# Kernel tuning notes

Hardware: AMD Instinct MI355X
Metric: run time of the kernel (lower is better)

## Reference

```python
import jax, jax.numpy as jnp
import numpy as np

# longformer-base-4096 config
L, H, D, DH, FF = 12, 12, 768, 64, 3072
B, S, W = 1, 4096, 256            # W = one-sided attention window (attention_window 512)
V, MAXP, NCLS = 50265, 4098, 6
NC = S // W                        # number of chunks of size W


def layer_norm(x, s, b, eps=1e-5):
    m = jnp.mean(x, -1, keepdims=True)
    v = jnp.var(x, -1, keepdims=True)
    return (x - m) * jax.lax.rsqrt(v + eps) * s + b


def sliding_attn(q, k, v, kv_mask):
    # q,k,v: [B,H,S,DH]; kv_mask: [B,S] float (1=keep, 0=pad)
    qc = q.reshape(B, H, NC, W, DH)
    pad = ((0, 0), (0, 0), (W, W), (0, 0))
    kp = jnp.pad(k, pad).reshape(B, H, NC + 2, W, DH)
    vp = jnp.pad(v, pad).reshape(B, H, NC + 2, W, DH)
    # each chunk c sees key chunks c-1, c, c+1 -> [B,H,NC,3W,DH]
    k3 = jnp.concatenate([kp[:, :, i:i + NC] for i in range(3)], axis=3)
    v3 = jnp.concatenate([vp[:, :, i:i + NC] for i in range(3)], axis=3)
    scores = jnp.einsum('bhcqd,bhckd->bhcqk', qc, k3) / np.float32(np.sqrt(DH))
    # banded mask: |key_global - query_global| <= W  <=>  qi <= kj <= qi + 2W
    qi = jnp.arange(W)[:, None]
    kj = jnp.arange(3 * W)[None, :]
    band = (kj >= qi) & (kj <= qi + 2 * W)                       # [W,3W]
    mp = jnp.pad(kv_mask, ((0, 0), (W, W))).reshape(B, NC + 2, W)
    m3 = jnp.concatenate([mp[:, i:i + NC] for i in range(3)], axis=2)  # [B,NC,3W]
    allowed = band[None, None, None] & (m3[:, None, :, None, :] > 0)
    probs = jax.nn.softmax(jnp.where(allowed, scores, -1e9), axis=-1)
    out = jnp.einsum('bhcqk,bhckd->bhcqd', probs, v3)            # [B,H,NC,W,DH]
    return out.reshape(B, H, S, DH)


def setup_inputs():
    ki = iter(jax.random.split(jax.random.key(0), 16))
    p = lambda sh: 0.02 * jax.random.normal(next(ki), sh, jnp.float32)
    ids = jax.random.randint(next(ki), (B, S), 0, V, dtype=jnp.int32)
    mask = jnp.ones((B, S), jnp.int32)
    return dict(
        ids=ids, mask=mask,
        word_emb=p((V, D)), pos_emb=p((MAXP, D)), type_emb=p((D,)),
        ln_e_s=jnp.ones((D,), jnp.float32), ln_e_b=jnp.zeros((D,), jnp.float32),
        wq=p((L, D, D)), bq=jnp.zeros((L, D), jnp.float32),
        wk=p((L, D, D)), bk=jnp.zeros((L, D), jnp.float32),
        wv=p((L, D, D)), bv=jnp.zeros((L, D), jnp.float32),
        wo=p((L, D, D)), bo=jnp.zeros((L, D), jnp.float32),
        ln1_s=jnp.ones((L, D), jnp.float32), ln1_b=jnp.zeros((L, D), jnp.float32),
        w1=p((L, D, FF)), b1=jnp.zeros((L, FF), jnp.float32),
        w2=p((L, FF, D)), b2=jnp.zeros((L, D), jnp.float32),
        ln2_s=jnp.ones((L, D), jnp.float32), ln2_b=jnp.zeros((L, D), jnp.float32),
        w_pool=p((D, D)), b_pool=jnp.zeros((D,), jnp.float32),
        w_cls=p((D, NCLS)), b_cls=jnp.zeros((NCLS,), jnp.float32))


def reference(ids, mask, word_emb, pos_emb, type_emb, ln_e_s, ln_e_b,
              wq, bq, wk, bk, wv, bv, wo, bo, ln1_s, ln1_b,
              w1, b1, w2, b2, ln2_s, ln2_b, w_pool, b_pool, w_cls, b_cls):
    maskf = mask.astype(jnp.float32)
    # RoBERTa-style position ids with padding_idx=1
    pos = (jnp.cumsum(mask, axis=1) * mask + 1).astype(jnp.int32)
    x = word_emb[ids] + pos_emb[pos] + type_emb               # [B,S,D]
    x = layer_norm(x, ln_e_s, ln_e_b)

    def heads(y, w, b):
        return (y @ w + b).reshape(B, S, H, DH).transpose(0, 2, 1, 3)

    for l in range(L):
        q = heads(x, wq[l], bq[l])
        k = heads(x, wk[l], bk[l])
        v = heads(x, wv[l], bv[l])
        a = sliding_attn(q, k, v, maskf)                      # [B,H,S,DH]
        a = a.transpose(0, 2, 1, 3).reshape(B, S, D)
        x = layer_norm(x + (a @ wo[l] + bo[l]), ln1_s[l], ln1_b[l])
        h = jax.nn.gelu(x @ w1[l] + b1[l], approximate=False)
        x = layer_norm(x + (h @ w2[l] + b2[l]), ln2_s[l], ln2_b[l])

    pooled = jnp.tanh(x[:, 0] @ w_pool + b_pool)              # [B,D] pooler
    # Dropout(0.3) is identity in eval mode
    return pooled @ w_cls + b_cls                             # [B,6]
```

## Files before the change

### kernel.cpp

```cpp
#include <hip/hip_runtime.h>
#include <stdint.h>
#include <math.h>

#define NL 12
#define SQ 4096
#define DM 768
#define NH 12
#define DHD 64
#define FF 3072
#define WW 256

typedef unsigned short u16;
typedef __attribute__((ext_vector_type(8))) short bf8_t;
typedef __attribute__((ext_vector_type(4))) short s16x4;
typedef __attribute__((ext_vector_type(4))) float f4;

__device__ __forceinline__ float bf2f(u16 h) {
  union { unsigned int u; float f; } c; c.u = ((unsigned int)h) << 16; return c.f;
}
__device__ __forceinline__ u16 f2bf(float f) {
  union { float f; unsigned int u; } c; c.f = f; unsigned int u = c.u;
  return (u16)((u + 0x7fffu + ((u >> 16) & 1u)) >> 16);
}
__device__ __forceinline__ int iclamp(int v, int lo, int hi) {
  return v < lo ? lo : (v > hi ? hi : v);
}
__device__ __forceinline__ void gload16(const void* g, void* l) {
  __builtin_amdgcn_global_load_lds(
      (const __attribute__((address_space(1))) void*)g,
      (__attribute__((address_space(3))) void*)l, 16, 0, 0);
}

__global__ __launch_bounds__(256) void scan_kernel(const int* __restrict__ mask,
                                                   int* __restrict__ pos) {
  __shared__ int part[256];
  int tid = threadIdx.x;
  int base = tid * 16, ssum = 0;
  for (int i = 0; i < 16; ++i) ssum += mask[base + i];
  part[tid] = ssum;
  __syncthreads();
  if (tid == 0) {
    int run = 0;
    for (int i = 0; i < 256; ++i) { int t = part[i]; part[i] = run; run += t; }
  }
  __syncthreads();
  int run = part[tid];
  for (int i = 0; i < 16; ++i) {
    int m = mask[base + i];
    run += m;
    pos[base + i] = run * m + 1;
  }
}

__device__ __forceinline__ void block_ln4(int row, f4 a, bool act,
    const float* __restrict__ s, const float* __restrict__ b,
    float* __restrict__ xo, u16* __restrict__ xh, float* red, int tid) {
  float s1 = 0.f, s2 = 0.f;
  if (act) {
#pragma unroll
    for (int j = 0; j < 4; ++j) { s1 += a[j]; s2 += a[j] * a[j]; }
  }
#pragma unroll
  for (int m = 1; m < 64; m <<= 1) { s1 += __shfl_xor(s1, m); s2 += __shfl_xor(s2, m); }
  if ((tid & 63) == 0) { red[tid >> 6] = s1; red[4 + (tid >> 6)] = s2; }
  __syncthreads();
  s1 = red[0] + red[1] + red[2] + red[3];
  s2 = red[4] + red[5] + red[6] + red[7];
  float mean = s1 * (1.f / DM);
  float var = s2 * (1.f / DM) - mean * mean;
  float inv = rsqrtf(var + 1e-5f);
  if (act) {
    const f4 sv = ((const f4*)s)[tid];
    const f4 bv = ((const f4*)b)[tid];
    f4 y;
    s16x4 hh;
#pragma unroll
    for (int j = 0; j < 4; ++j) {
      y[j] = (a[j] - mean) * inv * sv[j] + bv[j];
      hh[j] = (short)f2bf(y[j]);
    }
    ((f4*)xo)[(size_t)row * 192 + tid] = y;
    *(s16x4*)&xh[(size_t)row * DM + tid * 4] = hh;
  }
}

__global__ __launch_bounds__(256) void embed_kernel(const int* __restrict__ ids,
    const int* __restrict__ pos, const float* __restrict__ we,
    const float* __restrict__ pe, const float* __restrict__ te,
    const float* __restrict__ s, const float* __restrict__ b,
    float* __restrict__ xo, u16* __restrict__ xh) {
  __shared__ float red[8];
  int row = blockIdx.x, tid = threadIdx.x;
  bool act = tid < 192;
  f4 a = { 0.f, 0.f, 0.f, 0.f };
  if (act) {
    int id = ids[row], pz = pos[row];
    const f4 wv = ((const f4*)we)[(size_t)id * 192 + tid];
    const f4 pv = ((const f4*)pe)[(size_t)pz * 192 + tid];
    const f4 tv = ((const f4*)te)[tid];
#pragma unroll
    for (int j = 0; j < 4; ++j) a[j] = wv[j] + pv[j] + tv[j];
  }
  block_ln4(row, a, act, s, b, xo, xh, red, tid);
}

__global__ __launch_bounds__(256) void ln_direct_kernel(
    const float* __restrict__ in, float* __restrict__ x, u16* __restrict__ xh,
    const float* __restrict__ s, const float* __restrict__ b) {
  __shared__ float red[8];
  int row = blockIdx.x, tid = threadIdx.x;
  bool act = tid < 192;
  f4 a = { 0.f, 0.f, 0.f, 0.f };
  if (act) a = ((const f4*)in)[(size_t)row * 192 + tid];
  block_ln4(row, a, act, s, b, x, xh, red, tid);
}

__global__ __launch_bounds__(256) void ln_fuse_kernel(
    const float* __restrict__ pp, int nparts, const float* __restrict__ bias,
    float* __restrict__ x, u16* __restrict__ xh,
    const float* __restrict__ s, const float* __restrict__ b) {
  __shared__ float red[8];
  int row = blockIdx.x, tid = threadIdx.x;
  bool act = tid < 192;
  f4 a = { 0.f, 0.f, 0.f, 0.f };
  if (act) {
    size_t i4 = (size_t)row * 192 + tid;
    a = ((const f4*)x)[i4];
    const f4 bb = ((const f4*)bias)[tid];
#pragma unroll
    for (int j = 0; j < 4; ++j) a[j] += bb[j];
    for (int p = 0; p < nparts; ++p) {
      const f4 pv = ((const f4*)pp)[(size_t)p * SQ * 192 + i4];
#pragma unroll
      for (int j = 0; j < 4; ++j) a[j] += pv[j];
    }
  }
  block_ln4(row, a, act, s, b, x, xh, red, tid);
}

__global__ __launch_bounds__(256) void wconv_all(
    const float* __restrict__ wq, const float* __restrict__ wk,
    const float* __restrict__ wv, const float* __restrict__ wo,
    const float* __restrict__ w1, const float* __restrict__ w2,
    u16* __restrict__ Wqkv, u16* __restrict__ Wo,
    u16* __restrict__ W1, u16* __restrict__ W2) {
  __shared__ float t[64 * 65];
  int b = blockIdx.x;
  int lay = blockIdx.y;
  const float* src;
  u16* dst;
  int K, N, rowoff, nx, tile;
  if (b < 216) {
    int j = b / 72;
    tile = b - j * 72;
    src = ((j == 0) ? wq : ((j == 1) ? wk : wv)) + (size_t)lay * DM * DM;
    dst = Wqkv + (size_t)lay * 3 * DM * DM;
    K = DM; N = DM; rowoff = j * DM; nx = 12;
  } else if (b < 288) {
    tile = b - 216;
    src = wo + (size_t)lay * DM * DM; dst = Wo + (size_t)lay * DM * DM;
    K = DM; N = DM; rowoff = 0; nx = 12;
  } else if (b < 576) {
    tile = b - 288;
    src = w1 + (size_t)lay * DM * FF; dst = W1 + (size_t)lay * DM * FF;
    K = DM; N = FF; rowoff = 0; nx = 48;
  } else {
    tile = b - 576;
    src = w2 + (size_t)lay * FF * DM; dst = W2 + (size_t)lay * FF * DM;
    K = FF; N = DM; rowoff = 0; nx = 12;
  }
  int n0 = (tile % nx) * 64, k0 = (tile / nx) * 128;
  int tid = threadIdx.x;
  int q = tid & 15, kr = tid >> 4;

  f4 v0[4], v1[4];
#pragma unroll
  for (int p = 0; p < 4; ++p)
    v0[p] = *(const f4*)&src[(size_t)(k0 + kr + p * 16) * N + n0 + q * 4];
#pragma unroll
  for (int p = 0; p < 4; ++p)
    v1[p] = *(const f4*)&src[(size_t)(k0 + 64 + kr + p * 16) * N + n0 + q * 4];

#pragma unroll
  for (int p = 0; p < 4; ++p) {
    int k = kr + p * 16;
#pragma unroll
    for (int j = 0; j < 4; ++j) t[k * 65 + q * 4 + j] = v0[p][j];
  }
  __syncthreads();
  {
    int n = tid >> 4, kq = (tid & 15) * 4;
#pragma unroll
    for (int c = 0; c < 4; ++c) {
      int nn = n + c * 16;
      s16x4 st;
#pragma unroll
      for (int i = 0; i < 4; ++i)
        st[i] = (short)f2bf(t[(kq + i) * 65 + nn]);
      *(s16x4*)&dst[(size_t)(rowoff + n0 + nn) * K + k0 + kq] = st;
    }
  }
  __syncthreads();
#pragma unroll
  for (int p = 0; p < 4; ++p) {
    int k = kr + p * 16;
#pragma unroll
    for (int j = 0; j < 4; ++j) t[k * 65 + q * 4 + j] = v1[p][j];
  }
  __syncthreads();
  {
    int n = tid >> 4, kq = (tid & 15) * 4;
#pragma unroll
    for (int c = 0; c < 4; ++c) {
      int nn = n + c * 16;
      s16x4 st;
#pragma unroll
      for (int i = 0; i < 4; ++i)
        st[i] = (short)f2bf(t[(kq + i) * 65 + nn]);
      *(s16x4*)&dst[(size_t)(rowoff + n0 + nn) * K + k0 + 64 + kq] = st;
    }
  }
}

template <int EPI>
__global__ __launch_bounds__(256, 3) void gemm1(
    const u16* __restrict__ A, const u16* __restrict__ B, int Kld, int ksl,
    int nx, int ntiles,
    const float* __restrict__ bias0, const float* __restrict__ bias1,
    const float* __restrict__ bias2, const float* __restrict__ resid,
    float* __restrict__ outf, u16* __restrict__ oh,
    u16* __restrict__ Qb, u16* __restrict__ Kb, u16* __restrict__ VTb) {
  __shared__ __align__(16) char smem[49152];

  const int tid = threadIdx.x;
  const int l = tid & 63;
  const int w = tid >> 6;
  const int lr = l & 15;
  const int lg = l >> 4;
  const int nwg = gridDim.x;
  const int bid = blockIdx.x;
  const int wg = (bid & 7) * (nwg >> 3) + (bid >> 3);
  const int part = wg / ntiles;
  const int t = wg - part * ntiles;
  const int bm = (t / nx) * 128;
  const int bn = (t % nx) * 64;
  const int k0 = part * ksl;
  const int wr = (w >> 1) * 64;
  const int wc = (w & 1) * 32;

  f4 acc[4][2];
  f4 z = { 0.f, 0.f, 0.f, 0.f };
#pragma unroll
  for (int i = 0; i < 4; ++i)
#pragma unroll
    for (int j = 0; j < 2; ++j) acc[i][j] = z;

  const int srow = tid >> 3;
  const int scol = ((tid & 7) * 8) ^ ((srow & 7) * 8);
  const int xw = (lr & 7) * 8;

  const int nkt = ksl >> 6;

  auto stage = [&](int slot, int kt) {
    int ksrc = k0 + (kt << 6);
    char* la = smem + slot * 24576 + (size_t)(tid & ~63) * 16;
    char* lb = la + 16384;
#pragma unroll
    for (int r = 0; r < 4; ++r)
      gload16(A + (size_t)(bm + srow + r * 32) * Kld + ksrc + scol, la + r * 4096);
#pragma unroll
    for (int r = 0; r < 2; ++r)
      gload16(B + (size_t)(bn + srow + r * 32) * Kld + ksrc + scol, lb + r * 4096);
  };

  stage(0, 0);
  stage(1, 1);
  asm volatile("s_waitcnt vmcnt(6)" ::: "memory");
  __builtin_amdgcn_s_barrier();
  __builtin_amdgcn_sched_barrier(0);

  for (int kt = 0; kt < nkt; ++kt) {
    const int cur = kt & 1;
    const u16* sA = (const u16*)(smem + cur * 24576);
    const u16* sB = sA + 8192;
#pragma unroll
    for (int ks = 0; ks < 2; ++ks) {
      bf8_t af[4], bfr[2];
#pragma unroll
      for (int mt = 0; mt < 4; ++mt)
        af[mt] = *(const bf8_t*)&sA[(wr + mt * 16 + lr) * 64 + ((ks * 32 + lg * 8) ^ xw)];
#pragma unroll
      for (int nt = 0; nt < 2; ++nt)
        bfr[nt] = *(const bf8_t*)&sB[(wc + nt * 16 + lr) * 64 + ((ks * 32 + lg * 8) ^ xw)];
#pragma unroll
      for (int mt = 0; mt < 4; ++mt)
#pragma unroll
        for (int nt = 0; nt < 2; ++nt)
          acc[mt][nt] = __builtin_amdgcn_mfma_f32_16x16x32_bf16(af[mt], bfr[nt], acc[mt][nt], 0, 0, 0);
    }
    asm volatile("s_waitcnt lgkmcnt(0)" ::: "memory");
    __builtin_amdgcn_sched_barrier(0);
    __builtin_amdgcn_s_barrier();
    if (kt + 2 < nkt) {
      stage(cur, kt + 2);
      asm volatile("s_waitcnt vmcnt(6)" ::: "memory");
    } else {
      asm volatile("s_waitcnt vmcnt(0)" ::: "memory");
    }
    __builtin_amdgcn_s_barrier();
    __builtin_amdgcn_sched_barrier(0);
  }
  __syncthreads();

  if constexpr (EPI == 3 || EPI == 4) {
#pragma unroll
    for (int mt = 0; mt < 4; ++mt)
#pragma unroll
      for (int nt = 0; nt < 2; ++nt) {
        int colg = bn + wc + nt * 16 + lr;
#pragma unroll
        for (int r = 0; r < 4; ++r) {
          int rowg = bm + wr + mt * 16 + lg * 4 + r;
          size_t idx = (size_t)rowg * DM + colg;
          if constexpr (EPI == 3) {
            outf[(size_t)part * SQ * DM + idx] = acc[mt][nt][r];
          } else {
            outf[idx] = acc[mt][nt][r] + bias0[colg] + resid[idx];
          }
        }
      }
    return;
  }

  float* ep = (float*)(smem + w * 9216);
  const int nbase = bn + wc;

  if constexpr (EPI == 0) {
    int tgt = nbase / DM;
    int within = nbase - tgt * DM;
    int head = within >> 6;
    const float* bp = (tgt == 0) ? bias0 : ((tgt == 1) ? bias1 : bias2);
    if (tgt == 2) {
#pragma unroll
      for (int mt = 0; mt < 4; ++mt)
#pragma unroll
        for (int nt = 0; nt < 2; ++nt) {
          int dh = (within & 63) + nt * 16 + lr;
          float bb = bp[within + nt * 16 + lr];
          int s0 = bm + wr + mt * 16 + lg * 4;
          s16x4 st;
#pragma unroll
          for (int r = 0; r < 4; ++r) st[r] = (short)f2bf(acc[mt][nt][r] + bb);
          *(s16x4*)&VTb[((size_t)(head * DHD + dh)) * SQ + s0] = st;
        }
    } else {
      u16* dst = (tgt == 0) ? Qb : Kb;
      float scale = (tgt == 0) ? 0.125f : 1.0f;
#pragma unroll
      for (int mt = 0; mt < 4; ++mt)
#pragma unroll
        for (int nt = 0; nt < 2; ++nt)
#pragma unroll
          for (int r = 0; r < 4; ++r)
            ep[(mt * 16 + lg * 4 + r) * 36 + nt * 16 + lr] = acc[mt][nt][r];
      asm volatile("s_waitcnt lgkmcnt(0)" ::: "memory");
      int coloff = (l & 7) * 4;
#pragma unroll
      for (int i = 0; i < 8; ++i) {
        int row = (l >> 3) + i * 8;
        int gs = bm + wr + row;
        f4 v = *(f4*)&ep[row * 36 + coloff];
        s16x4 st;
#pragma unroll
        for (int j = 0; j < 4; ++j)
          st[j] = (short)f2bf((v[j] + bp[within + coloff + j]) * scale);
        *(s16x4*)&dst[((size_t)head * SQ + gs) * DHD + (within & 63) + coloff] = st;
      }
    }
  } else {
#pragma unroll
    for (int mt = 0; mt < 4; ++mt)
#pragma unroll
      for (int nt = 0; nt < 2; ++nt)
#pragma unroll
        for (int r = 0; r < 4; ++r)
          ep[(mt * 16 + lg * 4 + r) * 36 + nt * 16 + lr] = acc[mt][nt][r];
    asm volatile("s_waitcnt lgkmcnt(0)" ::: "memory");
    int coloff = (l & 7) * 4;
#pragma unroll
    for (int i = 0; i < 8; ++i) {
      int row = (l >> 3) + i * 8;
      int gs = bm + wr + row;
      f4 v = *(f4*)&ep[row * 36 + coloff];
      s16x4 hi;
#pragma unroll
      for (int j = 0; j < 4; ++j) {
        float t2 = v[j] + bias0[nbase + coloff + j];
        t2 = 0.5f * t2 * (1.f + erff(t2 * 0.70710678118654752f));
        hi[j] = (short)f2bf(t2);
      }
      *(s16x4*)&oh[(size_t)gs * FF + nbase + coloff] = hi;
    }
  }
}

__global__ __launch_bounds__(128) void attn_kernel(
    const u16* __restrict__ Qb, const u16* __restrict__ Kb,
    const u16* __restrict__ VTb, const int* __restrict__ mask,
    u16* __restrict__ ah) {
  __shared__ __align__(16) u16 Pl[2][32 * 72];
  __shared__ float mwin[640];
  const int tid = threadIdx.x;
  const int w = tid >> 6;
  const int l = tid & 63;
  const int lr = l & 15, lg = l >> 4;
  const int h = blockIdx.y;
  const int q0 = blockIdx.x * 64;
  const int qw = q0 + w * 32;
  const int kbw = qw - 256;
  for (int i = tid; i < 640; i += 128) {
    int kg = q0 - 256 + i;
    mwin[i] = (kg >= 0 && kg < SQ && mask[kg] != 0) ? 1.f : 0.f;
  }
  __syncthreads();
  u16* Plw = Pl[w];

  bf8_t qf[2][2];
#pragma unroll
  for (int mt = 0; mt < 2; ++mt)
#pragma unroll
    for (int ks = 0; ks < 2; ++ks)
      qf[mt][ks] = *(const bf8_t*)&Qb[((size_t)h * SQ + qw + mt * 16 + lr) * DHD + ks * 32 + lg * 8];

  f4 o[2][4];
  f4 z = { 0.f, 0.f, 0.f, 0.f };
  float mrow[2][4], lrow[2][4];
#pragma unroll
  for (int mt = 0; mt < 2; ++mt)
#pragma unroll
    for (int nt = 0; nt < 4; ++nt) o[mt][nt] = z;
#pragma unroll
  for (int mt = 0; mt < 2; ++mt)
#pragma unroll
    for (int r = 0; r < 4; ++r) { mrow[mt][r] = -1e30f; lrow[mt][r] = 0.f; }

  for (int kc = 0; kc < 9; ++kc) {
    int klb = kc * 64;
    int mo = w * 32 + klb;
    f4 sc[2][4];
#pragma unroll
    for (int mt = 0; mt < 2; ++mt)
#pragma unroll
      for (int nt = 0; nt < 4; ++nt) sc[mt][nt] = z;
#pragma unroll
    for (int ks = 0; ks < 2; ++ks) {
      bf8_t kf[4];
#pragma unroll
      for (int nt = 0; nt < 4; ++nt) {
        int krow = iclamp(kbw + klb + nt * 16 + lr, 0, SQ - 1);
        kf[nt] = *(const bf8_t*)&Kb[((size_t)h * SQ + krow) * DHD + ks * 32 + lg * 8];
      }
#pragma unroll
      for (int mt = 0; mt < 2; ++mt)
#pragma unroll
        for (int nt = 0; nt < 4; ++nt)
          sc[mt][nt] = __builtin_amdgcn_mfma_f32_16x16x32_bf16(qf[mt][ks], kf[nt], sc[mt][nt], 0, 0, 0);
    }
    bool edge = (kc == 0) | (kc == 8);
    unsigned long long vb = __ballot(mwin[mo + l] > 0.5f);
    if (edge || vb != ~0ull) {
#pragma unroll
      for (int mt = 0; mt < 2; ++mt)
#pragma unroll
        for (int nt = 0; nt < 4; ++nt) {
          int col = nt * 16 + lr;
          int kg = kbw + klb + col;
          float mk = mwin[mo + col];
#pragma unroll
          for (int r = 0; r < 4; ++r) {
            int qg = qw + mt * 16 + lg * 4 + r;
            int d = kg - qg;
            bool ok = (mk > 0.5f) && (!edge || ((d <= WW) && (d >= -WW)));
            sc[mt][nt][r] = ok ? sc[mt][nt][r] : -3.0e38f;
          }
        }
    }
#pragma unroll
    for (int mt = 0; mt < 2; ++mt)
#pragma unroll
      for (int r = 0; r < 4; ++r) {
        float cm = fmaxf(fmaxf(sc[mt][0][r], sc[mt][1][r]),
                         fmaxf(sc[mt][2][r], sc[mt][3][r]));
#pragma unroll
        for (int m2 = 1; m2 < 16; m2 <<= 1) cm = fmaxf(cm, __shfl_xor(cm, m2));
        float mn = fmaxf(fmaxf(mrow[mt][r], cm), -1e30f);
        float scl = __expf(mrow[mt][r] - mn);
        mrow[mt][r] = mn;
        float ps = 0.f;
#pragma unroll
        for (int nt = 0; nt < 4; ++nt) {
          float pv = __expf(sc[mt][nt][r] - mn);
          sc[mt][nt][r] = pv;
          ps += pv;
        }
#pragma unroll
        for (int m2 = 1; m2 < 16; m2 <<= 1) ps += __shfl_xor(ps, m2);
        lrow[mt][r] = lrow[mt][r] * scl + ps;
#pragma unroll
        for (int nt = 0; nt < 4; ++nt) o[mt][nt][r] *= scl;
#pragma unroll
        for (int nt = 0; nt < 4; ++nt)
          Plw[(mt * 16 + lg * 4 + r) * 72 + nt * 16 + lr] = f2bf(sc[mt][nt][r]);
      }
    asm volatile("s_waitcnt lgkmcnt(0)" ::: "memory");
#pragma unroll
    for (int ks = 0; ks < 2; ++ks) {
      bf8_t pa[2], vf[4];
#pragma unroll
      for (int mt = 0; mt < 2; ++mt)
        pa[mt] = *(const bf8_t*)&Plw[(mt * 16 + lr) * 72 + ks * 32 + lg * 8];
      int kbase = iclamp(kbw + klb + ks * 32 + lg * 8, 0, SQ - 8);
#pragma unroll
      for (int nt = 0; nt < 4; ++nt)
        vf[nt] = *(const bf8_t*)&VTb[((size_t)h * DHD + nt * 16 + lr) * SQ + kbase];
#pragma unroll
      for (int mt = 0; mt < 2; ++mt)
#pragma unroll
        for (int nt = 0; nt < 4; ++nt)
          o[mt][nt] = __builtin_amdgcn_mfma_f32_16x16x32_bf16(pa[mt], vf[nt], o[mt][nt], 0, 0, 0);
    }
  }
#pragma unroll
  for (int mt = 0; mt < 2; ++mt)
#pragma unroll
    for (int nt = 0; nt < 4; ++nt) {
      int col = h * DHD + nt * 16 + lr;
#pragma unroll
      for (int r = 0; r < 4; ++r) {
        int gq = qw + mt * 16 + lg * 4 + r;
        float v = o[mt][nt][r] / lrow[mt][r];
        ah[(size_t)gq * DM + col] = f2bf(v);
      }
    }
}

__global__ __launch_bounds__(256) void head1_kernel(const float* __restrict__ x,
    const float* __restrict__ wp, const float* __restrict__ bp,
    float* __restrict__ y) {
  __shared__ float x0[DM];
  __shared__ float part[4][64];
  int tid = threadIdx.x;
  int w = tid >> 6, l = tid & 63;
  for (int i = tid; i < DM; i += 256) x0[i] = x[i];
  __syncthreads();
  int j = blockIdx.x * 64 + l;
  float a = 0.f;
  int i0 = w * 192;
#pragma unroll 4
  for (int i = i0; i < i0 + 192; ++i) a += x0[i] * wp[(size_t)i * DM + j];
  part[w][l] = a;
  __syncthreads();
  if (w == 0) {
    float t = part[0][l] + part[1][l] + part[2][l] + part[3][l] + bp[j];
    y[j] = tanhf(t);
  }
}

__global__ __launch_bounds__(64) void head2_kernel(const float* __restrict__ y,
    const float* __restrict__ wc, const float* __restrict__ bc,
    float* __restrict__ out) {
  int l = threadIdx.x;
  float acc[6] = {0.f, 0.f, 0.f, 0.f, 0.f, 0.f};
  for (int i = l; i < DM; i += 64) {
    float yv = y[i];
#pragma unroll
    for (int j = 0; j < 6; ++j) acc[j] += yv * wc[i * 6 + j];
  }
#pragma unroll
  for (int j = 0; j < 6; ++j)
#pragma unroll
    for (int m = 1; m < 64; m <<= 1) acc[j] += __shfl_xor(acc[j], m);
  if (l == 0) {
#pragma unroll
    for (int j = 0; j < 6; ++j) out[j] = acc[j] + bc[j];
  }
}

extern "C" void kernel_launch(void* const* d_in, const int* in_sizes, int n_in,
                              void* d_out, int out_size, void* d_ws, size_t ws_size,
                              hipStream_t stream) {
  const int* ids = (const int*)d_in[0];
  const int* mask = (const int*)d_in[1];
  const float* we = (const float*)d_in[2];
  const float* pe = (const float*)d_in[3];
  const float* te = (const float*)d_in[4];
  const float* ln_e_s = (const float*)d_in[5];
  const float* ln_e_b = (const float*)d_in[6];
  const float* wq = (const float*)d_in[7];
  const float* bq = (const float*)d_in[8];
  const float* wk = (const float*)d_in[9];
  const float* bk = (const float*)d_in[10];
  const float* wv = (const float*)d_in[11];
  const float* bv = (const float*)d_in[12];
  const float* wo = (const float*)d_in[13];
  const float* bo = (const float*)d_in[14];
  const float* ln1_s = (const float*)d_in[15];
  const float* ln1_b = (const float*)d_in[16];
  const float* w1 = (const float*)d_in[17];
  const float* b1 = (const float*)d_in[18];
  const float* w2 = (const float*)d_in[19];
  const float* b2 = (const float*)d_in[20];
  const float* ln2_s = (const float*)d_in[21];
  const float* ln2_b = (const float*)d_in[22];
  const float* wpool = (const float*)d_in[23];
  const float* bpool = (const float*)d_in[24];
  const float* wcls = (const float*)d_in[25];
  const float* bcls = (const float*)d_in[26];

  char* p = (char*)d_ws;
  auto take = [&](size_t bytes) {
    char* r = p;
    p += (bytes + 255) & ~(size_t)255;
    return r;
  };
  int* pos = (int*)take((size_t)SQ * 4);
  float* x = (float*)take((size_t)SQ * DM * 4);
  float* pp = (float*)take((size_t)2 * SQ * DM * 4);
  u16* xh = (u16*)take((size_t)SQ * DM * 2);
  u16* Wqkv_h = (u16*)take((size_t)NL * 3 * DM * DM * 2);
  u16* Wo_h = (u16*)take((size_t)NL * DM * DM * 2);
  u16* W1_h = (u16*)take((size_t)NL * DM * FF * 2);
  u16* W2_h = (u16*)take((size_t)NL * FF * DM * 2);
  u16* Qb = (u16*)take((size_t)NH * SQ * DHD * 2);
  u16* Kbf = (u16*)take((size_t)NH * SQ * DHD * 2);
  u16* VTb = (u16*)take((size_t)NH * DHD * SQ * 2);
  u16* ah_ = (u16*)take((size_t)SQ * DM * 2);
  u16* hh = (u16*)take((size_t)SQ * FF * 2);
  float* ypool = (float*)take((size_t)DM * 4);

  scan_kernel<<<dim3(1), dim3(256), 0, stream>>>(mask, pos);
  embed_kernel<<<dim3(SQ), dim3(256), 0, stream>>>(ids, pos, we, pe, te, ln_e_s, ln_e_b, x, xh);
  wconv_all<<<dim3(864, NL), dim3(256), 0, stream>>>(
      wq, wk, wv, wo, w1, w2, Wqkv_h, Wo_h, W1_h, W2_h);

  for (int l = 0; l < NL; ++l) {
    const u16* Wq_l = Wqkv_h + (size_t)l * 3 * DM * DM;
    const u16* Wo_l = Wo_h + (size_t)l * DM * DM;
    const u16* W1_l = W1_h + (size_t)l * DM * FF;
    const u16* W2_l = W2_h + (size_t)l * FF * DM;

    gemm1<0><<<dim3(1152), dim3(256), 0, stream>>>(
        xh, Wq_l, DM, DM, 36, 1152, bq + (size_t)l * DM, bk + (size_t)l * DM,
        bv + (size_t)l * DM, nullptr, nullptr, nullptr, Qb, Kbf, VTb);
    attn_kernel<<<dim3(SQ / 64, NH), dim3(128), 0, stream>>>(Qb, Kbf, VTb, mask, ah_);
    gemm1<4><<<dim3(384), dim3(256), 0, stream>>>(
        ah_, Wo_l, DM, DM, 12, 384, bo + (size_t)l * DM, nullptr, nullptr, x,
        pp, nullptr, nullptr, nullptr, nullptr);
    ln_direct_kernel<<<dim3(SQ), dim3(256), 0, stream>>>(
        pp, x, xh, ln1_s + (size_t)l * DM, ln1_b + (size_t)l * DM);
    gemm1<2><<<dim3(1536), dim3(256), 0, stream>>>(
        xh, W1_l, DM, DM, 48, 1536, b1 + (size_t)l * FF, nullptr, nullptr, nullptr,
        nullptr, hh, nullptr, nullptr, nullptr);
    gemm1<3><<<dim3(768), dim3(256), 0, stream>>>(
        hh, W2_l, FF, FF / 2, 12, 384, nullptr, nullptr, nullptr, nullptr,
        pp, nullptr, nullptr, nullptr, nullptr);
    ln_fuse_kernel<<<dim3(SQ), dim3(256), 0, stream>>>(
        pp, 2, b2 + (size_t)l * DM, x, xh, ln2_s + (size_t)l * DM, ln2_b + (size_t)l * DM);
  }

  head1_kernel<<<dim3(12), dim3(256), 0, stream>>>(x, wpool, bpool, ypool);
  head2_kernel<<<dim3(1), dim3(64), 0, stream>>>(ypool, wcls, bcls, (float*)d_out);
}
```

Baseline: 2.181 ms.

## Prefetch next K tile and V tile early in sliding-window attention; split weight conversion launches

```diff
diff --git a/kernel.cpp b/kernel.cpp
--- a/kernel.cpp
+++ b/kernel.cpp
@@ -143,10 +143,10 @@
     const float* __restrict__ wv, const float* __restrict__ wo,
     const float* __restrict__ w1, const float* __restrict__ w2,
     u16* __restrict__ Wqkv, u16* __restrict__ Wo,
-    u16* __restrict__ W1, u16* __restrict__ W2) {
+    u16* __restrict__ W1, u16* __restrict__ W2, int lay0) {
   __shared__ float t[64 * 65];
   int b = blockIdx.x;
-  int lay = blockIdx.y;
+  int lay = blockIdx.y + lay0;
   const float* src;
   u16* dst;
   int K, N, rowoff, nx, tile;
@@ -444,6 +444,15 @@
 #pragma unroll
     for (int r = 0; r < 4; ++r) { mrow[mt][r] = -1e30f; lrow[mt][r] = 0.f; }
 
+  bf8_t kf[2][4];
+#pragma unroll
+  for (int ks = 0; ks < 2; ++ks)
+#pragma unroll
+    for (int nt = 0; nt < 4; ++nt) {
+      int krow = iclamp(kbw + nt * 16 + lr, 0, SQ - 1);
+      kf[ks][nt] = *(const bf8_t*)&Kb[((size_t)h * SQ + krow) * DHD + ks * 32 + lg * 8];
+    }
+
   for (int kc = 0; kc < 9; ++kc) {
     int klb = kc * 64;
     int mo = w * 32 + klb;
@@ -453,19 +462,33 @@
 #pragma unroll
       for (int nt = 0; nt < 4; ++nt) sc[mt][nt] = z;
 #pragma unroll
+    for (int ks = 0; ks < 2; ++ks)
+#pragma unroll
+      for (int mt = 0; mt < 2; ++mt)
+#pragma unroll
+        for (int nt = 0; nt < 4; ++nt)
+          sc[mt][nt] = __builtin_amdgcn_mfma_f32_16x16x32_bf16(qf[mt][ks], kf[ks][nt], sc[mt][nt], 0, 0, 0);
+
+    bf8_t vf[2][4];
+#pragma unroll
     for (int ks = 0; ks < 2; ++ks) {
-      bf8_t kf[4];
-#pragma unroll
-      for (int nt = 0; nt < 4; ++nt) {
-        int krow = iclamp(kbw + klb + nt * 16 + lr, 0, SQ - 1);
-        kf[nt] = *(const bf8_t*)&Kb[((size_t)h * SQ + krow) * DHD + ks * 32 + lg * 8];
-      }
-#pragma unroll
-      for (int mt = 0; mt < 2; ++mt)
-#pragma unroll
-        for (int nt = 0; nt < 4; ++nt)
-          sc[mt][nt] = __builtin_amdgcn_mfma_f32_16x16x32_bf16(qf[mt][ks], kf[nt], sc[mt][nt], 0, 0, 0);
-    }
+      int kbase = iclamp(kbw + klb + ks * 32 + lg * 8, 0, SQ - 8);
+#pragma unroll
+      for (int nt = 0; nt < 4; ++nt)
+        vf[ks][nt] = *(const bf8_t*)&VTb[((size_t)h * DHD + nt * 16 + lr) * SQ + kbase];
+    }
+    bf8_t kfn[2][4];
+    if (kc + 1 < 9) {
+      int klb2 = klb + 64;
+#pragma unroll
+      for (int ks = 0; ks < 2; ++ks)
+#pragma unroll
+        for (int nt = 0; nt < 4; ++nt) {
+          int krow = iclamp(kbw + klb2 + nt * 16 + lr, 0, SQ - 1);
+          kfn[ks][nt] = *(const bf8_t*)&Kb[((size_t)h * SQ + krow) * DHD + ks * 32 + lg * 8];
+        }
+    }
+
     bool edge = (kc == 0) | (kc == 8);
     unsigned long long vb = __ballot(mwin[mo + l] > 0.5f);
     if (edge || vb != ~0ull) {
@@ -515,19 +538,21 @@
     asm volatile("s_waitcnt lgkmcnt(0)" ::: "memory");
 #pragma unroll
     for (int ks = 0; ks < 2; ++ks) {
-      bf8_t pa[2], vf[4];
+      bf8_t pa[2];
 #pragma unroll
       for (int mt = 0; mt < 2; ++mt)
         pa[mt] = *(const bf8_t*)&Plw[(mt * 16 + lr) * 72 + ks * 32 + lg * 8];
-      int kbase = iclamp(kbw + klb + ks * 32 + lg * 8, 0, SQ - 8);
-#pragma unroll
-      for (int nt = 0; nt < 4; ++nt)
-        vf[nt] = *(const bf8_t*)&VTb[((size_t)h * DHD + nt * 16 + lr) * SQ + kbase];
 #pragma unroll
       for (int mt = 0; mt < 2; ++mt)
 #pragma unroll
         for (int nt = 0; nt < 4; ++nt)
-          o[mt][nt] = __builtin_amdgcn_mfma_f32_16x16x32_bf16(pa[mt], vf[nt], o[mt][nt], 0, 0, 0);
+          o[mt][nt] = __builtin_amdgcn_mfma_f32_16x16x32_bf16(pa[mt], vf[ks][nt], o[mt][nt], 0, 0, 0);
+    }
+    if (kc + 1 < 9) {
+#pragma unroll
+      for (int ks = 0; ks < 2; ++ks)
+#pragma unroll
+        for (int nt = 0; nt < 4; ++nt) kf[ks][nt] = kfn[ks][nt];
     }
   }
 #pragma unroll
@@ -640,8 +665,9 @@
 
   scan_kernel<<<dim3(1), dim3(256), 0, stream>>>(mask, pos);
   embed_kernel<<<dim3(SQ), dim3(256), 0, stream>>>(ids, pos, we, pe, te, ln_e_s, ln_e_b, x, xh);
-  wconv_all<<<dim3(864, NL), dim3(256), 0, stream>>>(
-      wq, wk, wv, wo, w1, w2, Wqkv_h, Wo_h, W1_h, W2_h);
+  for (int sl = 0; sl < 4; ++sl)
+    wconv_all<<<dim3(864, 3), dim3(256), 0, stream>>>(
+        wq, wk, wv, wo, w1, w2, Wqkv_h, Wo_h, W1_h, W2_h, sl * 3);
 
   for (int l = 0; l < NL; ++l) {
     const u16* Wq_l = Wqkv_h + (size_t)l * 3 * DM * DM;
```

After: 2.293 ms. 5.2% more time.

## Use 128x128 tile GEMM kernel for QKV and FFN-up projections

Applied to the files above, without the earlier changes.

```diff
diff --git a/kernel.cpp b/kernel.cpp
--- a/kernel.cpp
+++ b/kernel.cpp
@@ -226,10 +226,8 @@
 __global__ __launch_bounds__(256, 3) void gemm1(
     const u16* __restrict__ A, const u16* __restrict__ B, int Kld, int ksl,
     int nx, int ntiles,
-    const float* __restrict__ bias0, const float* __restrict__ bias1,
-    const float* __restrict__ bias2, const float* __restrict__ resid,
-    float* __restrict__ outf, u16* __restrict__ oh,
-    u16* __restrict__ Qb, u16* __restrict__ Kb, u16* __restrict__ VTb) {
+    const float* __restrict__ bias0, const float* __restrict__ resid,
+    float* __restrict__ outf) {
   __shared__ __align__(16) char smem[49152];
 
   const int tid = threadIdx.x;
@@ -312,24 +310,98 @@
   }
   __syncthreads();
 
-  if constexpr (EPI == 3 || EPI == 4) {
-#pragma unroll
-    for (int mt = 0; mt < 4; ++mt)
-#pragma unroll
-      for (int nt = 0; nt < 2; ++nt) {
-        int colg = bn + wc + nt * 16 + lr;
-#pragma unroll
-        for (int r = 0; r < 4; ++r) {
-          int rowg = bm + wr + mt * 16 + lg * 4 + r;
-          size_t idx = (size_t)rowg * DM + colg;
-          if constexpr (EPI == 3) {
-            outf[(size_t)part * SQ * DM + idx] = acc[mt][nt][r];
-          } else {
-            outf[idx] = acc[mt][nt][r] + bias0[colg] + resid[idx];
-          }
+#pragma unroll
+  for (int mt = 0; mt < 4; ++mt)
+#pragma unroll
+    for (int nt = 0; nt < 2; ++nt) {
+      int colg = bn + wc + nt * 16 + lr;
+#pragma unroll
+      for (int r = 0; r < 4; ++r) {
+        int rowg = bm + wr + mt * 16 + lg * 4 + r;
+        size_t idx = (size_t)rowg * DM + colg;
+        if constexpr (EPI == 3) {
+          outf[(size_t)part * SQ * DM + idx] = acc[mt][nt][r];
+        } else {
+          outf[idx] = acc[mt][nt][r] + bias0[colg] + resid[idx];
         }
       }
-    return;
+    }
+}
+
+template <int EPI>
+__global__ __launch_bounds__(256, 3) void gemm2(
+    const u16* __restrict__ A, const u16* __restrict__ B, int Kld, int ksl,
+    int nx,
+    const float* __restrict__ bias0, const float* __restrict__ bias1,
+    const float* __restrict__ bias2,
+    u16* __restrict__ oh, u16* __restrict__ Qb, u16* __restrict__ Kb,
+    u16* __restrict__ VTb) {
+  __shared__ __align__(16) char smem[36864];
+
+  const int tid = threadIdx.x;
+  const int l = tid & 63;
+  const int w = tid >> 6;
+  const int lr = l & 15;
+  const int lg = l >> 4;
+  const int nwg = gridDim.x;
+  const int bid = blockIdx.x;
+  const int wg = (bid & 7) * (nwg >> 3) + (bid >> 3);
+  const int bm = (wg / nx) * 128;
+  const int bn = (wg % nx) * 128;
+  const int wr = (w >> 1) * 64;
+  const int wc = (w & 1) * 64;
+
+  f4 acc[4][4];
+  f4 z = { 0.f, 0.f, 0.f, 0.f };
+#pragma unroll
+  for (int i = 0; i < 4; ++i)
+#pragma unroll
+    for (int j = 0; j < 4; ++j) acc[i][j] = z;
+
+  const int srow = tid >> 3;
+  const int scol = ((tid & 7) * 8) ^ ((srow & 7) * 8);
+  const int xw = (lr & 7) * 8;
+
+  const int nkt = ksl >> 6;
+
+  auto stage = [&](int kt) {
+    int ksrc = kt << 6;
+    char* la = smem + (size_t)(tid & ~63) * 16;
+    char* lb = la + 16384;
+#pragma unroll
+    for (int r = 0; r < 4; ++r)
+      gload16(A + (size_t)(bm + srow + r * 32) * Kld + ksrc + scol, la + r * 4096);
+#pragma unroll
+    for (int r = 0; r < 4; ++r)
+      gload16(B + (size_t)(bn + srow + r * 32) * Kld + ksrc + scol, lb + r * 4096);
+  };
+
+  stage(0);
+  for (int kt = 0; kt < nkt; ++kt) {
+    asm volatile("s_waitcnt vmcnt(0)" ::: "memory");
+    __builtin_amdgcn_s_barrier();
+    __builtin_amdgcn_sched_barrier(0);
+    const u16* sA = (const u16*)smem;
+    const u16* sB = sA + 8192;
+#pragma unroll
+    for (int ks = 0; ks < 2; ++ks) {
+      bf8_t af[4], bfr[4];
+#pragma unroll
+      for (int mt = 0; mt < 4; ++mt)
+        af[mt] = *(const bf8_t*)&sA[(wr + mt * 16 + lr) * 64 + ((ks * 32 + lg * 8) ^ xw)];
+#pragma unroll
+      for (int nt = 0; nt < 4; ++nt)
+        bfr[nt] = *(const bf8_t*)&sB[(wc + nt * 16 + lr) * 64 + ((ks * 32 + lg * 8) ^ xw)];
+#pragma unroll
+      for (int mt = 0; mt < 4; ++mt)
+#pragma unroll
+        for (int nt = 0; nt < 4; ++nt)
+          acc[mt][nt] = __builtin_amdgcn_mfma_f32_16x16x32_bf16(af[mt], bfr[nt], acc[mt][nt], 0, 0, 0);
+    }
+    asm volatile("s_waitcnt lgkmcnt(0)" ::: "memory");
+    __builtin_amdgcn_sched_barrier(0);
+    __builtin_amdgcn_s_barrier();
+    if (kt + 1 < nkt) stage(kt + 1);
   }
 
   float* ep = (float*)(smem + w * 9216);
@@ -344,9 +416,9 @@
 #pragma unroll
       for (int mt = 0; mt < 4; ++mt)
 #pragma unroll
-        for (int nt = 0; nt < 2; ++nt) {
-          int dh = (within & 63) + nt * 16 + lr;
-          float bb = bp[within + nt * 16 + lr];
+        for (int nt = 0; nt < 4; ++nt) {
+          int dh = nt * 16 + lr;
+          float bb = bp[within + dh];
           int s0 = bm + wr + mt * 16 + lg * 4;
           s16x4 st;
 #pragma unroll
@@ -356,50 +428,58 @@
     } else {
       u16* dst = (tgt == 0) ? Qb : Kb;
       float scale = (tgt == 0) ? 0.125f : 1.0f;
+      int coloff = (l & 7) * 4;
+#pragma unroll
+      for (int half = 0; half < 2; ++half) {
+        if (half) asm volatile("s_waitcnt lgkmcnt(0)" ::: "memory");
+#pragma unroll
+        for (int mt = 0; mt < 4; ++mt)
+#pragma unroll
+          for (int n2 = 0; n2 < 2; ++n2)
+#pragma unroll
+            for (int r = 0; r < 4; ++r)
+              ep[(mt * 16 + lg * 4 + r) * 36 + n2 * 16 + lr] = acc[mt][half * 2 + n2][r];
+        asm volatile("s_waitcnt lgkmcnt(0)" ::: "memory");
+#pragma unroll
+        for (int i = 0; i < 8; ++i) {
+          int row = (l >> 3) + i * 8;
+          int gs = bm + wr + row;
+          f4 v = *(f4*)&ep[row * 36 + coloff];
+          s16x4 st;
+#pragma unroll
+          for (int j = 0; j < 4; ++j)
+            st[j] = (short)f2bf((v[j] + bp[within + half * 32 + coloff + j]) * scale);
+          *(s16x4*)&dst[((size_t)head * SQ + gs) * DHD + half * 32 + coloff] = st;
+        }
+      }
+    }
+  } else {
+    int coloff = (l & 7) * 4;
+#pragma unroll
+    for (int half = 0; half < 2; ++half) {
+      if (half) asm volatile("s_waitcnt lgkmcnt(0)" ::: "memory");
 #pragma unroll
       for (int mt = 0; mt < 4; ++mt)
 #pragma unroll
-        for (int nt = 0; nt < 2; ++nt)
+        for (int n2 = 0; n2 < 2; ++n2)
 #pragma unroll
           for (int r = 0; r < 4; ++r)
-            ep[(mt * 16 + lg * 4 + r) * 36 + nt * 16 + lr] = acc[mt][nt][r];
+            ep[(mt * 16 + lg * 4 + r) * 36 + n2 * 16 + lr] = acc[mt][half * 2 + n2][r];
       asm volatile("s_waitcnt lgkmcnt(0)" ::: "memory");
-      int coloff = (l & 7) * 4;
 #pragma unroll
       for (int i = 0; i < 8; ++i) {
         int row = (l >> 3) + i * 8;
         int gs = bm + wr + row;
         f4 v = *(f4*)&ep[row * 36 + coloff];
-        s16x4 st;
-#pragma unroll
-        for (int j = 0; j < 4; ++j)
-          st[j] = (short)f2bf((v[j] + bp[within + coloff + j]) * scale);
-        *(s16x4*)&dst[((size_t)head * SQ + gs) * DHD + (within & 63) + coloff] = st;
+        s16x4 hi;
+#pragma unroll
+        for (int j = 0; j < 4; ++j) {
+          float t2 = v[j] + bias0[nbase + half * 32 + coloff + j];
+          t2 = 0.5f * t2 * (1.f + erff(t2 * 0.70710678118654752f));
+          hi[j] = (short)f2bf(t2);
+        }
+        *(s16x4*)&oh[(size_t)gs * FF + nbase + half * 32 + coloff] = hi;
       }
-    }
-  } else {
-#pragma unroll
-    for (int mt = 0; mt < 4; ++mt)
-#pragma unroll
-      for (int nt = 0; nt < 2; ++nt)
-#pragma unroll
-        for (int r = 0; r < 4; ++r)
-          ep[(mt * 16 + lg * 4 + r) * 36 + nt * 16 + lr] = acc[mt][nt][r];
-    asm volatile("s_waitcnt lgkmcnt(0)" ::: "memory");
-    int coloff = (l & 7) * 4;
-#pragma unroll
-    for (int i = 0; i < 8; ++i) {
-      int row = (l >> 3) + i * 8;
-      int gs = bm + wr + row;
-      f4 v = *(f4*)&ep[row * 36 + coloff];
-      s16x4 hi;
-#pragma unroll
-      for (int j = 0; j < 4; ++j) {
-        float t2 = v[j] + bias0[nbase + coloff + j];
-        t2 = 0.5f * t2 * (1.f + erff(t2 * 0.70710678118654752f));
-        hi[j] = (short)f2bf(t2);
-      }
-      *(s16x4*)&oh[(size_t)gs * FF + nbase + coloff] = hi;
     }
   }
 }
@@ -649,21 +729,19 @@
     const u16* W1_l = W1_h + (size_t)l * DM * FF;
     const u16* W2_l = W2_h + (size_t)l * FF * DM;
 
-    gemm1<0><<<dim3(1152), dim3(256), 0, stream>>>(
-        xh, Wq_l, DM, DM, 36, 1152, bq + (size_t)l * DM, bk + (size_t)l * DM,
-        bv + (size_t)l * DM, nullptr, nullptr, nullptr, Qb, Kbf, VTb);
+    gemm2<0><<<dim3(576), dim3(256), 0, stream>>>(
+        xh, Wq_l, DM, DM, 18, bq + (size_t)l * DM, bk + (size_t)l * DM,
+        bv + (size_t)l * DM, nullptr, Qb, Kbf, VTb);
     attn_kernel<<<dim3(SQ / 64, NH), dim3(128), 0, stream>>>(Qb, Kbf, VTb, mask, ah_);
     gemm1<4><<<dim3(384), dim3(256), 0, stream>>>(
-        ah_, Wo_l, DM, DM, 12, 384, bo + (size_t)l * DM, nullptr, nullptr, x,
-        pp, nullptr, nullptr, nullptr, nullptr);
+        ah_, Wo_l, DM, DM, 12, 384, bo + (size_t)l * DM, x, pp);
     ln_direct_kernel<<<dim3(SQ), dim3(256), 0, stream>>>(
         pp, x, xh, ln1_s + (size_t)l * DM, ln1_b + (size_t)l * DM);
-    gemm1<2><<<dim3(1536), dim3(256), 0, stream>>>(
-        xh, W1_l, DM, DM, 48, 1536, b1 + (size_t)l * FF, nullptr, nullptr, nullptr,
-        nullptr, hh, nullptr, nullptr, nullptr);
+    gemm2<2><<<dim3(768), dim3(256), 0, stream>>>(
+        xh, W1_l, DM, DM, 24, b1 + (size_t)l * FF, nullptr, nullptr,
+        hh, nullptr, nullptr, nullptr);
     gemm1<3><<<dim3(768), dim3(256), 0, stream>>>(
-        hh, W2_l, FF, FF / 2, 12, 384, nullptr, nullptr, nullptr, nullptr,
-        pp, nullptr, nullptr, nullptr, nullptr);
+        hh, W2_l, FF, FF / 2, 12, 384, nullptr, nullptr, pp);
     ln_fuse_kernel<<<dim3(SQ), dim3(256), 0, stream>>>(
         pp, 2, b2 + (size_t)l * DM, x, xh, ln2_s + (size_t)l * DM, ln2_b + (size_t)l * DM);
   }
```

After: 2.112 ms. -3.2%, faster.
